# Kernel tuning notes

Measured on AMD Instinct MI355X. Metric: run time of the kernel, lower is better.

Reference implementation:

```python
import jax, jax.numpy as jnp
import numpy as np
from jax import lax

B, T, D, H, C, FF, NH = 256, 48, 89, 128, 64, 64, 8
HD = C // NH


def _pos_encoding(n, c):
    pos = jnp.arange(n, dtype=jnp.float32)[:, None]
    div = jnp.exp(jnp.arange(0, c, 2, dtype=jnp.float32) * (-np.log(10000.0) / c))
    pe = jnp.zeros((n, c), dtype=jnp.float32)
    pe = pe.at[:, 0::2].set(jnp.sin(pos * div))
    pe = pe.at[:, 1::2].set(jnp.cos(pos * div))
    return pe


def _ln(x, g, b):
    m = x.mean(-1, keepdims=True)
    v = ((x - m) ** 2).mean(-1, keepdims=True)
    return (x - m) / jnp.sqrt(v + 1e-5) * g + b


def setup_inputs():
    key = jax.random.key(0)
    ks = iter(jax.random.split(key, 64))
    def n(shape, s=0.05):
        return (jax.random.normal(next(ks), shape) * s).astype(jnp.float32)
    x = jax.random.normal(next(ks), (B, T, D), dtype=jnp.float32)
    mask = (jax.random.uniform(next(ks), (B, T, D)) < 0.8).astype(jnp.float32)
    deltas = (jax.random.uniform(next(ks), (B, T, D)) * 5.0).astype(jnp.float32)
    last_obs = jax.random.normal(next(ks), (B, T, D), dtype=jnp.float32)
    medians = (jax.random.uniform(next(ks), (D,)) * 2.0).astype(jnp.float32)
    return dict(
        x=x, mask=mask, deltas=deltas, last_obs=last_obs, medians=medians,
        W_dh=n((H, D)), b_dh=n((H,)), W_dx=n((D, D)), b_dx=n((D,)),
        W_hist=n((D, H)), b_hist=n((D,)), W_feat=n((D, D)), b_feat=n((D,)),
        W_wc=n((D, 2 * D)), b_wc=n((D,)), W_wo=n((D, D)), b_wo=n((D,)),
        W_cls=n((1, H)), b_cls=n((1,)),
        W_ih=n((3 * H, 2 * D)), W_hh=n((3 * H, H)), b_ih=n((3 * H,)), b_hh=n((3 * H,)),
        W_inp=n((C, D)), b_inp=n((C,)), W_op1=n((H, C)), b_op1=n((H,)),
        W_op2=n((2 * T,)), b_op2=n((1,)),
        attn_in_w=n((3 * C, C)), attn_in_b=n((3 * C,)),
        attn_out_w=n((C, C)), attn_out_b=n((C,)),
        ln1_g=jnp.ones((C,)), ln1_b=jnp.zeros((C,)),
        ln2_g=jnp.ones((C,)), ln2_b=jnp.zeros((C,)),
        ff1_w=n((FF, C)), ff1_b=n((FF,)), ff2_w=n((C, FF)), ff2_b=n((C,)))


def _forward(x, mask, deltas, last_obs, medians,
             W_dh, b_dh, W_dx, b_dx, W_hist, b_hist, W_feat, b_feat,
             W_wc, b_wc, W_wo, b_wo, W_cls, b_cls,
             W_ih, W_hh, b_ih, b_hh, W_inp, b_inp, W_op1, b_op1, W_op2, b_op2,
             attn_in_w, attn_in_b, attn_out_w, attn_out_b,
             ln1_g, ln1_b, ln2_g, ln2_b, ff1_w, ff1_b, ff2_w, ff2_b):
    # Decay_obs: weight = 0.5*(1 - tanh(sign(dd)*|linear(dd)|))
    dd = deltas - medians[None, None, :]
    wd = dd @ W_wo.T + b_wo
    decay_factor = 0.5 * (1.0 - jnp.tanh(jnp.sign(dd) * jnp.abs(wd)))

    # time encoder: 1x1 conv projection + positional encoding
    pe = _pos_encoding(T, C)[None]                      # [1,T,C]
    d_lo = last_obs @ W_inp.T + b_inp + pe              # [B,T,C]
    d_df = decay_factor @ W_inp.T + b_inp + pe          # [B,T,C]
    data = jnp.concatenate([d_lo, d_df], axis=1)        # [B,2T,C]

    # torch TransformerEncoderLayer (post-norm, gelu, dropout off).
    # NOTE: layer is NOT batch_first, so attention runs over axis 0 (B);
    # axis 1 (2T) behaves as the batch — faithful to the source.
    qkv = data @ attn_in_w.T + attn_in_b                # [B,2T,3C]
    q, k, v = jnp.split(qkv, 3, axis=-1)
    q = q.reshape(B, 2 * T, NH, HD)
    k = k.reshape(B, 2 * T, NH, HD)
    v = v.reshape(B, 2 * T, NH, HD)
    scores = jnp.einsum('snhd,tnhd->nhst', q, k) / np.sqrt(HD)
    probs = jax.nn.softmax(scores, axis=-1)
    o = jnp.einsum('nhst,tnhd->snhd', probs, v).reshape(B, 2 * T, C)
    o = o @ attn_out_w.T + attn_out_b
    x1 = _ln(data + o, ln1_g, ln1_b)
    ff = jax.nn.gelu(x1 @ ff1_w.T + ff1_b, approximate=False) @ ff2_w.T + ff2_b
    data = _ln(x1 + ff, ln2_g, ln2_b)                   # [B,2T,C]

    data = data @ W_op1.T + b_op1                       # [B,2T,H]
    h0 = jnp.einsum('bnh,n->bh', data, W_op2) + b_op2[0]  # Conv1d(2T->1,k=1)

    diag_w = jnp.diagonal(W_dx)                         # temp_decay_x diag mask
    offdiag = 1.0 - jnp.eye(D, dtype=x.dtype)

    def step(carry, inp):
        h, loss = carry
        x_t, m_t, d_t = inp
        gamma_h = jnp.exp(-jax.nn.relu(d_t @ W_dh.T + b_dh))
        h = h * gamma_h
        x_h = h @ W_hist.T + b_hist
        x_r = m_t * x_t + (1.0 - m_t) * x_h
        xu = x_r @ (W_feat * offdiag).T + b_feat
        gamma_x = jnp.exp(-jax.nn.relu(d_t * diag_w + b_dx))
        beta = jnp.concatenate([gamma_x, m_t], axis=-1) @ W_wc.T + b_wc
        x_comb = beta * xu + (1.0 - beta) * x_h
        loss = loss + jnp.sum(jnp.abs(x_t - x_comb) * m_t) / (jnp.sum(m_t) + 1e-5)
        x_imp_t = m_t * x_t + (1.0 - m_t) * x_comb
        gi = jnp.concatenate([x_imp_t, m_t], axis=-1) @ W_ih.T + b_ih
        gh = h @ W_hh.T + b_hh
        ir, iz, ig = jnp.split(gi, 3, axis=-1)
        hr, hz, hg = jnp.split(gh, 3, axis=-1)
        r = jax.nn.sigmoid(ir + hr)
        z = jax.nn.sigmoid(iz + hz)
        g = jnp.tanh(ig + r * hg)
        h = (1.0 - z) * g + z * h
        return (h, loss), (x_imp_t, h)

    xs = (x.transpose(1, 0, 2), mask.transpose(1, 0, 2), deltas.transpose(1, 0, 2))
    (h, x_loss), (x_imp_T, hid_T) = lax.scan(step, (h0, jnp.zeros((), x.dtype)), xs)
    x_imp = x_imp_T.transpose(1, 0, 2)                  # [B,T,D]
    hiddens = hid_T.transpose(1, 0, 2)                  # [B,T,H]

    y_out = h @ W_cls.T + b_cls
    y_score = jax.nn.sigmoid(y_out)
    return x_imp, x_loss, hiddens, y_out, y_score


def reference(x, mask, deltas, last_obs, medians,
              W_dh, b_dh, W_dx, b_dx, W_hist, b_hist, W_feat, b_feat,
              W_wc, b_wc, W_wo, b_wo, W_cls, b_cls,
              W_ih, W_hh, b_ih, b_hh, W_inp, b_inp, W_op1, b_op1, W_op2, b_op2,
              attn_in_w, attn_in_b, attn_out_w, attn_out_b,
              ln1_g, ln1_b, ln2_g, ln2_b, ff1_w, ff1_b, ff2_w, ff2_b):
    return _forward(x, mask, deltas, last_obs, medians,
                    W_dh, b_dh, W_dx, b_dx, W_hist, b_hist, W_feat, b_feat,
                    W_wc, b_wc, W_wo, b_wo, W_cls, b_cls,
                    W_ih, W_hh, b_ih, b_hh, W_inp, b_inp, W_op1, b_op1, W_op2, b_op2,
                    attn_in_w, attn_in_b, attn_out_w, attn_out_b,
                    ln1_g, ln1_b, ln2_g, ln2_b, ff1_w, ff1_b, ff2_w, ff2_b)
```

## Files before the change

### kernel.cpp

```cpp
#include <hip/hip_runtime.h>
#include <math.h>

#define B_  256
#define T_  48
#define D_  89
#define H_  128
#define C_  64
#define NH_ 8
#define HD_ 8
#define N2T 96

#define XIMP_OFF 0
#define LOSS_OFF 1093632
#define HID_OFF  1093633
#define Y_OFF    2666497
#define YS_OFF   2666753

typedef unsigned int uint_t;

__device__ __forceinline__ float wave_sum64(float v) {
    v += __shfl_xor(v, 32);
    v += __shfl_xor(v, 16);
    v += __shfl_xor(v, 8);
    v += __shfl_xor(v, 4);
    v += __shfl_xor(v, 2);
    v += __shfl_xor(v, 1);
    return v;
}

__device__ __forceinline__ uint_t pack2(float lo, float hi) {
    uint_t a = __float_as_uint(lo), b = __float_as_uint(hi);
    a = (a + 0x7fffu + ((a >> 16) & 1u)) >> 16;
    b = (b + 0x7fffu + ((b >> 16) & 1u)) >> 16;
    return a | (b << 16);
}
__device__ __forceinline__ float blo(uint_t w) { return __uint_as_float(w << 16); }
__device__ __forceinline__ float bhi(uint_t w) { return __uint_as_float(w & 0xffff0000u); }
__device__ __forceinline__ float sigm(float v) { return 1.f / (1.f + __expf(-v)); }

__device__ __forceinline__ void tr_f32(const float* __restrict__ s, float* __restrict__ d,
                                       int li, int R, int C) {
    int r = li / C, c = li - r * C;
    d[c * R + r] = s[li];
}

__global__ void k_prep(const float* W_wo, const float* W_inp, const float* ain_w,
                       const float* aout_w, const float* ff1_w, const float* ff2_w,
                       const float* W_op1,
                       float* W_woT, float* W_inpT, float* ain_T,
                       float* aout_T, float* ff1_T, float* ff2_T, float* op1_T) {
    int i = blockIdx.x * 256 + threadIdx.x;
    if (i < 7921)         tr_f32(W_wo,   W_woT,  i,          89, 89);
    else if (i < 13617)   tr_f32(W_inp,  W_inpT, i - 7921,   64, 89);
    else if (i < 25905)   tr_f32(ain_w,  ain_T,  i - 13617, 192, 64);
    else if (i < 30001)   tr_f32(aout_w, aout_T, i - 25905,  64, 64);
    else if (i < 34097)   tr_f32(ff1_w,  ff1_T,  i - 30001,  64, 64);
    else if (i < 38193)   tr_f32(ff2_w,  ff2_T,  i - 34097,  64, 64);
    else if (i < 46385)   tr_f32(W_op1,  op1_T,  i - 38193, 128, 64);
}

__global__ void k_pack(const float* __restrict__ W_dh, const float* __restrict__ W_hist,
                       const float* __restrict__ W_ih, const float* __restrict__ W_hh,
                       uint_t* __restrict__ wdh_b, uint_t* __restrict__ whist_b,
                       uint_t* __restrict__ wih_b, uint_t* __restrict__ whh_b) {
    int i = blockIdx.x * 256 + threadIdx.x;
    if (i < 5760) {
        int r = i / 45, c = i - r * 45;
        const float* src = W_dh + r * 89;
        float lo = (2 * c < 89) ? src[2 * c] : 0.f;
        float hi = (2 * c + 1 < 89) ? src[2 * c + 1] : 0.f;
        wdh_b[i] = pack2(lo, hi);
    } else if (i < 11456) {
        int j = i - 5760;
        int r = j / 64, c = j - r * 64;
        const float* src = W_hist + r * 128;
        whist_b[j] = pack2(src[2 * c], src[2 * c + 1]);
    } else if (i < 45632) {
        int j = i - 11456;
        int r = j / 89, c = j - r * 89;
        const float* src = W_ih + (size_t)r * 178;
        wih_b[j] = pack2(src[2 * c], src[2 * c + 1]);
    } else if (i < 70208) {
        int j = i - 45632;
        int r = j / 64, c = j - r * 64;
        const float* src = W_hh + (size_t)r * 128;
        whh_b[j] = pack2(src[2 * c], src[2 * c + 1]);
    }
}

__global__ void k_phaseA(const float* __restrict__ last_obs,
                         const float* __restrict__ deltas,
                         const float* __restrict__ medians,
                         const float* __restrict__ W_woT, const float* __restrict__ b_wo,
                         const float* __restrict__ W_inpT, const float* __restrict__ b_inp,
                         float* __restrict__ data) {
    int bt = blockIdx.x;
    int b = bt / T_;
    int t = bt - b * T_;
    __shared__ float dd[D_], lo[D_], dec[D_];
    int tid = threadIdx.x;
    int base = (b * T_ + t) * D_;
    if (tid < D_) {
        float dv = deltas[base + tid] - medians[tid];
        dd[tid] = dv;
        lo[tid] = last_obs[base + tid];
    }
    __syncthreads();
    if (tid < D_) {
        float acc = b_wo[tid];
        for (int j = 0; j < D_; ++j) acc = fmaf(dd[j], W_woT[j * D_ + tid], acc);
        float dv = dd[tid];
        float s = (dv > 0.f) ? 1.f : ((dv < 0.f) ? -1.f : 0.f);
        dec[tid] = 0.5f * (1.f - tanhf(s * fabsf(acc)));
    }
    __syncthreads();
    int c = tid & 63;
    int half = tid >> 6;
    const float* src = half ? dec : lo;
    float acc = b_inp[c];
    for (int j = 0; j < D_; ++j) acc = fmaf(src[j], W_inpT[j * C_ + c], acc);
    int i = c >> 1;
    float div = __expf((float)i * -0.28782313662425574f);
    float ang = (float)t * div;
    float pe = (c & 1) ? cosf(ang) : sinf(ang);
    data[((b * N2T) + half * T_ + t) * C_ + c] = acc + pe;
}

__global__ void k_qkv(const float* __restrict__ data,
                      const float* __restrict__ ain_T, const float* __restrict__ ain_b,
                      float* __restrict__ qb, float* __restrict__ kb, float* __restrict__ vb) {
    int bn = blockIdx.x;
    int s = bn / N2T;
    int n = bn - s * N2T;
    __shared__ float row[C_];
    int tid = threadIdx.x;
    if (tid < C_) row[tid] = data[bn * C_ + tid];
    __syncthreads();
    float acc = ain_b[tid];
    for (int j = 0; j < C_; ++j) acc = fmaf(row[j], ain_T[j * 192 + tid], acc);
    int part = tid >> 6;
    int c = tid & 63;
    int h = c >> 3, d = c & 7;
    float* dst = (part == 0) ? qb : ((part == 1) ? kb : vb);
    dst[(((n * NH_ + h) * B_ + s) * HD_) + d] = acc;
}

__global__ void k_attn(const float* __restrict__ qb, const float* __restrict__ kb,
                       const float* __restrict__ vb, float* __restrict__ attnO) {
    int n = blockIdx.x >> 3;
    int h = blockIdx.x & 7;
    __shared__ float k_lds[B_][HD_ + 1];
    __shared__ float v_lds[B_][HD_ + 1];
    int s = threadIdx.x;
    const float scale = 0.35355339059327373f;
    size_t base = ((size_t)blockIdx.x * B_ + s) * HD_;
    float q[HD_];
    #pragma unroll
    for (int d = 0; d < HD_; ++d) q[d] = qb[base + d] * scale;
    #pragma unroll
    for (int d = 0; d < HD_; ++d) { k_lds[s][d] = kb[base + d]; v_lds[s][d] = vb[base + d]; }
    __syncthreads();
    float m = -1e30f;
    for (int t = 0; t < B_; ++t) {
        float sc = 0.f;
        #pragma unroll
        for (int d = 0; d < HD_; ++d) sc = fmaf(q[d], k_lds[t][d], sc);
        m = fmaxf(m, sc);
    }
    float l = 0.f;
    float acc[HD_] = {0.f, 0.f, 0.f, 0.f, 0.f, 0.f, 0.f, 0.f};
    for (int t = 0; t < B_; ++t) {
        float sc = 0.f;
        #pragma unroll
        for (int d = 0; d < HD_; ++d) sc = fmaf(q[d], k_lds[t][d], sc);
        float p = __expf(sc - m);
        l += p;
        #pragma unroll
        for (int d = 0; d < HD_; ++d) acc[d] = fmaf(p, v_lds[t][d], acc[d]);
    }
    float inv = 1.f / l;
    float* op = attnO + ((size_t)s * N2T + n) * C_ + h * HD_;
    #pragma unroll
    for (int d = 0; d < HD_; ++d) op[d] = acc[d] * inv;
}

__global__ void k_transform(const float* __restrict__ data,
                            const float* __restrict__ attnO,
                            const float* __restrict__ aout_T, const float* __restrict__ aout_b,
                            const float* __restrict__ ln1_g, const float* __restrict__ ln1_b,
                            const float* __restrict__ ff1_T, const float* __restrict__ ff1_b,
                            const float* __restrict__ ff2_T, const float* __restrict__ ff2_b,
                            const float* __restrict__ ln2_g, const float* __restrict__ ln2_b,
                            const float* __restrict__ op1_T, const float* __restrict__ b_op1,
                            float* __restrict__ val) {
    int bn = blockIdx.x;
    __shared__ float orow[C_], x1s[C_], hbuf[C_], x2s[C_];
    int c = threadIdx.x;
    float d0 = data[bn * C_ + c];
    orow[c] = attnO[bn * C_ + c];
    __syncthreads();
    float acc = aout_b[c];
    for (int j = 0; j < C_; ++j) acc = fmaf(orow[j], aout_T[j * C_ + c], acc);
    float r = d0 + acc;
    float mean = wave_sum64(r) * (1.f / 64.f);
    float df = r - mean;
    float var = wave_sum64(df * df) * (1.f / 64.f);
    float x1 = df * rsqrtf(var + 1e-5f) * ln1_g[c] + ln1_b[c];
    x1s[c] = x1;
    __syncthreads();
    acc = ff1_b[c];
    for (int j = 0; j < C_; ++j) acc = fmaf(x1s[j], ff1_T[j * C_ + c], acc);
    float ge = 0.5f * acc * (1.f + erff(acc * 0.7071067811865475f));
    hbuf[c] = ge;
    __syncthreads();
    acc = ff2_b[c];
    for (int j = 0; j < C_; ++j) acc = fmaf(hbuf[j], ff2_T[j * C_ + c], acc);
    float r2 = x1 + acc;
    float mean2 = wave_sum64(r2) * (1.f / 64.f);
    float df2 = r2 - mean2;
    float var2 = wave_sum64(df2 * df2) * (1.f / 64.f);
    float x2 = df2 * rsqrtf(var2 + 1e-5f) * ln2_g[c] + ln2_b[c];
    x2s[c] = x2;
    __syncthreads();
    #pragma unroll
    for (int rep = 0; rep < 2; ++rep) {
        int k = c + rep * 64;
        float a2 = b_op1[k];
        for (int j = 0; j < C_; ++j) a2 = fmaf(x2s[j], op1_T[j * H_ + k], a2);
        val[(size_t)bn * H_ + k] = a2;
    }
}

__global__ void k_reduce_h0(const float* __restrict__ val,
                            const float* __restrict__ W_op2, const float* __restrict__ b_op2,
                            float* __restrict__ h0) {
    int b = blockIdx.x;
    int h = threadIdx.x;
    float acc = b_op2[0];
    for (int n = 0; n < N2T; ++n)
        acc = fmaf(val[((size_t)b * N2T + n) * H_ + h], W_op2[n], acc);
    h0[b * H_ + h] = acc;
}

__global__ void k_den(const float* __restrict__ mask, float* __restrict__ den) {
    int t = blockIdx.x;
    int tid = threadIdx.x;
    float s = 0.f;
    const int total = B_ * D_;
    for (int i = tid; i < total; i += 256) {
        int b = i / D_;
        int d = i - b * D_;
        s += mask[(b * T_ + t) * D_ + d];
    }
    s = wave_sum64(s);
    __shared__ float red[4];
    if ((tid & 63) == 0) red[tid >> 6] = s;
    __syncthreads();
    if (tid == 0) den[t] = red[0] + red[1] + red[2] + red[3];
}

__global__ __launch_bounds__(1024)
void k_scan(const float* __restrict__ x, const float* __restrict__ mask,
            const float* __restrict__ deltas,
            const uint_t* __restrict__ wdh_b, const float* __restrict__ b_dh,
            const float* __restrict__ W_dx, const float* __restrict__ b_dx,
            const uint_t* __restrict__ whist_b, const float* __restrict__ b_hist,
            const float* __restrict__ W_feat, const float* __restrict__ b_feat,
            const float* __restrict__ W_wc, const float* __restrict__ b_wc,
            const uint_t* __restrict__ wih_b, const uint_t* __restrict__ whh_b,
            const float* __restrict__ b_ih, const float* __restrict__ b_hh,
            const float* __restrict__ W_cls, const float* __restrict__ b_cls,
            const float* __restrict__ h0,
            float* __restrict__ out, float* __restrict__ num_part) {
    int b = blockIdx.x;
    int tid = threadIdx.x;
    int wave = tid >> 6;
    int lane = tid & 63;
    int oo = lane >> 3;
    int jj = lane & 7;

    __shared__ __align__(16) float h_s[H_];
    __shared__ __align__(16) float xt_s[96], dt_s[96], xr_s[96], xh_s[96], diff_s[96];
    __shared__ __align__(16) float catg_s[184];
    __shared__ __align__(16) float catb_s[184];
    __shared__ __align__(16) float gis[384], ghs[384];
    __shared__ __align__(16) uint_t wwc_l[7921];
    __shared__ __align__(16) uint_t wfeat_l[4005];

    for (int i = tid; i < 7921; i += 1024) {
        int r = i / 89, c = i - r * 89;
        const float* wr = W_wc + (size_t)r * 178;
        wwc_l[i] = pack2(wr[2 * c], wr[2 * c + 1]);
    }
    for (int i = tid; i < 4005; i += 1024) {
        int r = i / 45, c = i - r * 45;
        const float* wr = W_feat + r * 89;
        float lo = (2 * c == r) ? 0.f : wr[2 * c];
        float hi = (c == 44 || 2 * c + 1 == r) ? 0.f : wr[2 * c + 1];
        wfeat_l[i] = pack2(lo, hi);
    }
    if (tid < 128) h_s[tid] = h0[b * H_ + tid];
    if (tid >= 512 && tid < 519) {
        int l = tid - 512;
        xr_s[89 + l] = 0.f;
        dt_s[89 + l] = 0.f;
    }
    {
        int base = b * T_ * D_;
        if (tid >= 128 && tid < 217) xt_s[tid - 128] = x[base + tid - 128];
        else if (tid >= 224 && tid < 313) {
            float m = mask[base + tid - 224];
            catg_s[89 + tid - 224] = m;
            catb_s[89 + tid - 224] = m;
        }
        else if (tid >= 320 && tid < 409) dt_s[tid - 320] = deltas[base + tid - 320];
    }
    __syncthreads();

    for (int t = 0; t < T_; ++t) {
        {
            int o = wave * 8 + oo;
            const uint_t* wr = wdh_b + o * 45;
            float a0 = 0.f, a1 = 0.f;
            #pragma unroll
            for (int it = 0; it < 5; ++it) {
                int j = jj + 8 * it;
                uint_t w = wr[j];
                float2 dv = *(const float2*)(dt_s + 2 * j);
                a0 = fmaf(blo(w), dv.x, a0);
                a1 = fmaf(bhi(w), dv.y, a1);
            }
            if (jj < 5) {
                int j = 40 + jj;
                uint_t w = wr[j];
                float2 dv = *(const float2*)(dt_s + 2 * j);
                a0 = fmaf(blo(w), dv.x, a0);
                a1 = fmaf(bhi(w), dv.y, a1);
            }
            float acc = a0 + a1;
            acc += __shfl_xor(acc, 1); acc += __shfl_xor(acc, 2); acc += __shfl_xor(acc, 4);
            if (jj == 0) h_s[o] *= __expf(-fmaxf(acc + b_dh[o], 0.f));
        }
        __syncthreads();
        for (int c = wave; c < 60; c += 16) {
            if (c < 12) {
                int o = c * 8 + oo;
                int ro = (o < 89) ? o : 88;
                const uint_t* wr = whist_b + ro * 64;
                float a0 = 0.f, a1 = 0.f;
                #pragma unroll
                for (int it = 0; it < 8; ++it) {
                    int j = jj + 8 * it;
                    uint_t w = wr[j];
                    float2 hv = *(const float2*)(h_s + 2 * j);
                    a0 = fmaf(blo(w), hv.x, a0);
                    a1 = fmaf(bhi(w), hv.y, a1);
                }
                float acc = a0 + a1;
                acc += __shfl_xor(acc, 1); acc += __shfl_xor(acc, 2); acc += __shfl_xor(acc, 4);
                if (jj == 0 && o < 89) {
                    float xh = acc + b_hist[o];
                    xh_s[o] = xh;
                    float m = catb_s[89 + o];
                    xr_s[o] = m * xt_s[o] + (1.f - m) * xh;
                    catb_s[o] = __expf(-fmaxf(dt_s[o] * W_dx[o * 90] + b_dx[o], 0.f));
                }
            } else {
                int o = (c - 12) * 8 + oo;
                const uint_t* wr = whh_b + o * 64;
                float a0 = 0.f, a1 = 0.f;
                #pragma unroll
                for (int it = 0; it < 8; ++it) {
                    int j = jj + 8 * it;
                    uint_t w = wr[j];
                    float2 hv = *(const float2*)(h_s + 2 * j);
                    a0 = fmaf(blo(w), hv.x, a0);
                    a1 = fmaf(bhi(w), hv.y, a1);
                }
                float acc = a0 + a1;
                acc += __shfl_xor(acc, 1); acc += __shfl_xor(acc, 2); acc += __shfl_xor(acc, 4);
                if (jj == 0) ghs[o] = acc + b_hh[o];
            }
        }
        __syncthreads();
        for (int c = wave; c < 12; c += 16) {
            int o = c * 8 + oo;
            int ro = (o < 89) ? o : 88;
            const uint_t* wf = wfeat_l + ro * 45;
            float a0 = 0.f, a1 = 0.f;
            #pragma unroll
            for (int it = 0; it < 5; ++it) {
                int j2 = jj + 8 * it;
                uint_t w = wf[j2];
                float2 xv = *(const float2*)(xr_s + 2 * j2);
                a0 = fmaf(blo(w), xv.x, a0);
                a1 = fmaf(bhi(w), xv.y, a1);
            }
            if (jj < 5) {
                int j2 = 40 + jj;
                uint_t w = wf[j2];
                float2 xv = *(const float2*)(xr_s + 2 * j2);
                a0 = fmaf(blo(w), xv.x, a0);
                a1 = fmaf(bhi(w), xv.y, a1);
            }
            float xu = a0 + a1;
            xu += __shfl_xor(xu, 1); xu += __shfl_xor(xu, 2); xu += __shfl_xor(xu, 4);
            const uint_t* wc = wwc_l + ro * 89;
            float c0 = 0.f, c1 = 0.f;
            #pragma unroll
            for (int it = 0; it < 11; ++it) {
                int j2 = jj + 8 * it;
                uint_t w = wc[j2];
                float2 cv = *(const float2*)(catb_s + 2 * j2);
                c0 = fmaf(blo(w), cv.x, c0);
                c1 = fmaf(bhi(w), cv.y, c1);
            }
            if (jj == 0) {
                uint_t w = wc[88];
                float2 cv = *(const float2*)(catb_s + 176);
                c0 = fmaf(blo(w), cv.x, c0);
                c1 = fmaf(bhi(w), cv.y, c1);
            }
            float bt = c0 + c1;
            bt += __shfl_xor(bt, 1); bt += __shfl_xor(bt, 2); bt += __shfl_xor(bt, 4);
            if (jj == 0 && o < 89) {
                float xuf = xu + b_feat[o];
                float btf = bt + b_wc[o];
                float xc = btf * xuf + (1.f - btf) * xh_s[o];
                float m = catb_s[89 + o];
                float xtv = xt_s[o];
                float xi = m * xtv + (1.f - m) * xc;
                catg_s[o] = xi;
                out[XIMP_OFF + (b * T_ + t) * D_ + o] = xi;
                diff_s[o] = fabsf(xtv - xc) * m;
            }
        }
        __syncthreads();
        for (int c = wave; c < 48; c += 16) {
            int o = c * 8 + oo;
            const uint_t* wr = wih_b + o * 89;
            float a0 = 0.f, a1 = 0.f;
            #pragma unroll
            for (int it = 0; it < 11; ++it) {
                int j = jj + 8 * it;
                uint_t w = wr[j];
                float2 xv = *(const float2*)(catg_s + 2 * j);
                a0 = fmaf(blo(w), xv.x, a0);
                a1 = fmaf(bhi(w), xv.y, a1);
            }
            if (jj == 0) {
                uint_t w = wr[88];
                float2 xv = *(const float2*)(catg_s + 176);
                a0 = fmaf(blo(w), xv.x, a0);
                a1 = fmaf(bhi(w), xv.y, a1);
            }
            float acc = a0 + a1;
            acc += __shfl_xor(acc, 1); acc += __shfl_xor(acc, 2); acc += __shfl_xor(acc, 4);
            if (jj == 0) gis[o] = acc + b_ih[o];
        }
        __syncthreads();
        if (tid < 128) {
            float r = sigm(gis[tid] + ghs[tid]);
            float z = sigm(gis[128 + tid] + ghs[128 + tid]);
            float g = tanhf(gis[256 + tid] + r * ghs[256 + tid]);
            float hn = (1.f - z) * g + z * h_s[tid];
            h_s[tid] = hn;
            out[HID_OFF + (size_t)(b * T_ + t) * H_ + tid] = hn;
        } else if (tid >= 960) {
            int l = tid - 960;
            float s = diff_s[l] + ((l < 25) ? diff_s[64 + l] : 0.f);
            s = wave_sum64(s);
            if (l == 0) num_part[t * B_ + b] = s;
        } else if (t + 1 < T_) {
            int nb = (b * T_ + t + 1) * D_;
            if (tid < 217) xt_s[tid - 128] = x[nb + tid - 128];
            else if (tid >= 224 && tid < 313) {
                float m = mask[nb + tid - 224];
                catg_s[89 + tid - 224] = m;
                catb_s[89 + tid - 224] = m;
            }
            else if (tid >= 320 && tid < 409) dt_s[tid - 320] = deltas[nb + tid - 320];
        }
        __syncthreads();
    }
    if (tid < 64) {
        float p = h_s[tid] * W_cls[tid] + h_s[tid + 64] * W_cls[tid + 64];
        p = wave_sum64(p);
        if (tid == 0) {
            float y = p + b_cls[0];
            out[Y_OFF + b] = y;
            out[YS_OFF + b] = 1.f / (1.f + __expf(-y));
        }
    }
}

__global__ void k_loss(const float* __restrict__ num_part, const float* __restrict__ den,
                       float* __restrict__ out) {
    int tid = threadIdx.x;
    float v = 0.f;
    if (tid < T_) {
        float s = 0.f;
        const float* np_ = num_part + tid * B_;
        for (int b = 0; b < B_; ++b) s += np_[b];
        v = s / (den[tid] + 1e-5f);
    }
    v = wave_sum64(v);
    if (tid == 0) out[LOSS_OFF] = v;
}

extern "C" void kernel_launch(void* const* d_in, const int* in_sizes, int n_in,
                              void* d_out, int out_size, void* d_ws, size_t ws_size,
                              hipStream_t stream) {
    const float* x        = (const float*)d_in[0];
    const float* mask     = (const float*)d_in[1];
    const float* deltas   = (const float*)d_in[2];
    const float* last_obs = (const float*)d_in[3];
    const float* medians  = (const float*)d_in[4];
    const float* W_dh  = (const float*)d_in[5];
    const float* b_dh  = (const float*)d_in[6];
    const float* W_dx  = (const float*)d_in[7];
    const float* b_dx  = (const float*)d_in[8];
    const float* W_hist= (const float*)d_in[9];
    const float* b_hist= (const float*)d_in[10];
    const float* W_feat= (const float*)d_in[11];
    const float* b_feat= (const float*)d_in[12];
    const float* W_wc  = (const float*)d_in[13];
    const float* b_wc  = (const float*)d_in[14];
    const float* W_wo  = (const float*)d_in[15];
    const float* b_wo  = (const float*)d_in[16];
    const float* W_cls = (const float*)d_in[17];
    const float* b_cls = (const float*)d_in[18];
    const float* W_ih  = (const float*)d_in[19];
    const float* W_hh  = (const float*)d_in[20];
    const float* b_ih  = (const float*)d_in[21];
    const float* b_hh  = (const float*)d_in[22];
    const float* W_inp = (const float*)d_in[23];
    const float* b_inp = (const float*)d_in[24];
    const float* W_op1 = (const float*)d_in[25];
    const float* b_op1 = (const float*)d_in[26];
    const float* W_op2 = (const float*)d_in[27];
    const float* b_op2 = (const float*)d_in[28];
    const float* attn_in_w  = (const float*)d_in[29];
    const float* attn_in_b  = (const float*)d_in[30];
    const float* attn_out_w = (const float*)d_in[31];
    const float* attn_out_b = (const float*)d_in[32];
    const float* ln1_g = (const float*)d_in[33];
    const float* ln1_b = (const float*)d_in[34];
    const float* ln2_g = (const float*)d_in[35];
    const float* ln2_b = (const float*)d_in[36];
    const float* ff1_w = (const float*)d_in[37];
    const float* ff1_b = (const float*)d_in[38];
    const float* ff2_w = (const float*)d_in[39];
    const float* ff2_b = (const float*)d_in[40];

    float* out = (float*)d_out;
    float* ws = (float*)d_ws;

    float* data  = ws;
    float* qb    = data  + (size_t)B_ * N2T * C_;
    float* kb    = qb    + (size_t)N2T * NH_ * B_ * HD_;
    float* vb    = kb    + (size_t)N2T * NH_ * B_ * HD_;
    float* attnO = vb    + (size_t)N2T * NH_ * B_ * HD_;
    float* val   = attnO + (size_t)B_ * N2T * C_;
    float* h0    = val   + (size_t)B_ * N2T * H_;
    float* den   = h0    + (size_t)B_ * H_;
    float* nump  = den   + 64;
    float* W_woT = nump  + T_ * B_;
    float* W_inpT= W_woT + 7921;
    float* ain_T = W_inpT + 5696;
    float* aout_T= ain_T + 12288;
    float* ff1_T = aout_T + 4096;
    float* ff2_T = ff1_T + 4096;
    float* op1_T = ff2_T + 4096;
    uint_t* wdh_b   = (uint_t*)(op1_T + 8192);
    uint_t* whist_b = wdh_b + 5760;
    uint_t* wih_b   = whist_b + 5696;
    uint_t* whh_b   = wih_b + 34176;

    k_prep<<<182, 256, 0, stream>>>(W_wo, W_inp, attn_in_w, attn_out_w, ff1_w, ff2_w, W_op1,
                                    W_woT, W_inpT, ain_T, aout_T, ff1_T, ff2_T, op1_T);
    k_pack<<<275, 256, 0, stream>>>(W_dh, W_hist, W_ih, W_hh, wdh_b, whist_b, wih_b, whh_b);
    k_phaseA<<<B_ * T_, 128, 0, stream>>>(last_obs, deltas, medians, W_woT, b_wo, W_inpT, b_inp, data);
    k_qkv<<<B_ * N2T, 192, 0, stream>>>(data, ain_T, attn_in_b, qb, kb, vb);
    k_attn<<<N2T * NH_, 256, 0, stream>>>(qb, kb, vb, attnO);
    k_transform<<<B_ * N2T, 64, 0, stream>>>(data, attnO, aout_T, attn_out_b,
                                             ln1_g, ln1_b, ff1_T, ff1_b, ff2_T, ff2_b,
                                             ln2_g, ln2_b, op1_T, b_op1, val);
    k_reduce_h0<<<B_, H_, 0, stream>>>(val, W_op2, b_op2, h0);
    k_den<<<T_, 256, 0, stream>>>(mask, den);
    k_scan<<<B_, 1024, 0, stream>>>(x, mask, deltas,
                                    wdh_b, b_dh, W_dx, b_dx, whist_b, b_hist, W_feat, b_feat,
                                    W_wc, b_wc, wih_b, whh_b, b_ih, b_hh, W_cls, b_cls,
                                    h0, out, nump);
    k_loss<<<1, 64, 0, stream>>>(nump, den, out);
}
```

Before: 625.9 us.

## Hoist mask/gamma-dependent GEMVs off the recurrence critical path in scan

The W_wc (beta) and the mask half of W_ih products depend only on the current step's mask and deltas, not on the hidden state. They now run in the first phase of each step, alongside the decay GEMV, instead of in the later serial phases. The gamma_x decay is computed while loading the next step's deltas. The later phases then only do the half-width W_ih product on the imputed values, shortening the dependent chain per timestep. The cost is more work in the first phase and a split W_ih layout with padding.

```diff
diff --git a/kernel.cpp b/kernel.cpp
--- a/kernel.cpp
+++ b/kernel.cpp
@@ -62,7 +62,8 @@
 __global__ void k_pack(const float* __restrict__ W_dh, const float* __restrict__ W_hist,
                        const float* __restrict__ W_ih, const float* __restrict__ W_hh,
                        uint_t* __restrict__ wdh_b, uint_t* __restrict__ whist_b,
-                       uint_t* __restrict__ wih_b, uint_t* __restrict__ whh_b) {
+                       uint_t* __restrict__ wihx_b, uint_t* __restrict__ wihm_b,
+                       uint_t* __restrict__ whh_b) {
     int i = blockIdx.x * 256 + threadIdx.x;
     if (i < 5760) {
         int r = i / 45, c = i - r * 45;
@@ -75,13 +76,22 @@
         int r = j / 64, c = j - r * 64;
         const float* src = W_hist + r * 128;
         whist_b[j] = pack2(src[2 * c], src[2 * c + 1]);
-    } else if (i < 45632) {
+    } else if (i < 28736) {
         int j = i - 11456;
-        int r = j / 89, c = j - r * 89;
+        int r = j / 45, c = j - r * 45;
         const float* src = W_ih + (size_t)r * 178;
-        wih_b[j] = pack2(src[2 * c], src[2 * c + 1]);
-    } else if (i < 70208) {
-        int j = i - 45632;
+        float lo = src[2 * c];
+        float hi = (2 * c + 1 < 89) ? src[2 * c + 1] : 0.f;
+        wihx_b[j] = pack2(lo, hi);
+    } else if (i < 46016) {
+        int j = i - 28736;
+        int r = j / 45, c = j - r * 45;
+        const float* src = W_ih + (size_t)r * 178 + 89;
+        float lo = src[2 * c];
+        float hi = (2 * c + 1 < 89) ? src[2 * c + 1] : 0.f;
+        wihm_b[j] = pack2(lo, hi);
+    } else if (i < 70592) {
+        int j = i - 46016;
         int r = j / 64, c = j - r * 64;
         const float* src = W_hh + (size_t)r * 128;
         whh_b[j] = pack2(src[2 * c], src[2 * c + 1]);
@@ -267,7 +277,8 @@
             const uint_t* __restrict__ whist_b, const float* __restrict__ b_hist,
             const float* __restrict__ W_feat, const float* __restrict__ b_feat,
             const float* __restrict__ W_wc, const float* __restrict__ b_wc,
-            const uint_t* __restrict__ wih_b, const uint_t* __restrict__ whh_b,
+            const uint_t* __restrict__ wihx_b, const uint_t* __restrict__ wihm_b,
+            const uint_t* __restrict__ whh_b,
             const float* __restrict__ b_ih, const float* __restrict__ b_hh,
             const float* __restrict__ W_cls, const float* __restrict__ b_cls,
             const float* __restrict__ h0,
@@ -280,66 +291,131 @@
     int jj = lane & 7;
 
     __shared__ __align__(16) float h_s[H_];
-    __shared__ __align__(16) float xt_s[96], dt_s[96], xr_s[96], xh_s[96], diff_s[96];
-    __shared__ __align__(16) float catg_s[184];
-    __shared__ __align__(16) float catb_s[184];
+    __shared__ __align__(16) float xt_s[96], dt_s[96], xr_s[96], xh_s[96];
+    __shared__ __align__(16) float m_s[96], gx_s[96], ximp_s[96], beta_s[96], diff_s[96];
     __shared__ __align__(16) float gis[384], ghs[384];
-    __shared__ __align__(16) uint_t wwc_l[7921];
+    __shared__ __align__(16) uint_t wwcg_l[4005];
+    __shared__ __align__(16) uint_t wwcm_l[4005];
     __shared__ __align__(16) uint_t wfeat_l[4005];
 
-    for (int i = tid; i < 7921; i += 1024) {
-        int r = i / 89, c = i - r * 89;
-        const float* wr = W_wc + (size_t)r * 178;
-        wwc_l[i] = pack2(wr[2 * c], wr[2 * c + 1]);
-    }
+    float dxw = 0.f, dxb = 0.f;
+    if (tid >= 320 && tid < 409) {
+        int o = tid - 320;
+        dxw = W_dx[o * 90];
+        dxb = b_dx[o];
+    }
+
     for (int i = tid; i < 4005; i += 1024) {
         int r = i / 45, c = i - r * 45;
-        const float* wr = W_feat + r * 89;
-        float lo = (2 * c == r) ? 0.f : wr[2 * c];
-        float hi = (c == 44 || 2 * c + 1 == r) ? 0.f : wr[2 * c + 1];
-        wfeat_l[i] = pack2(lo, hi);
+        const float* wr = W_wc + (size_t)r * 178;
+        float lo = wr[2 * c];
+        float hi = (2 * c + 1 < 89) ? wr[2 * c + 1] : 0.f;
+        wwcg_l[i] = pack2(lo, hi);
+        const float* wm = wr + 89;
+        float lo2 = wm[2 * c];
+        float hi2 = (2 * c + 1 < 89) ? wm[2 * c + 1] : 0.f;
+        wwcm_l[i] = pack2(lo2, hi2);
+        const float* wf = W_feat + r * 89;
+        float lo3 = (2 * c == r) ? 0.f : wf[2 * c];
+        float hi3 = (2 * c + 1 >= 89 || 2 * c + 1 == r) ? 0.f : wf[2 * c + 1];
+        wfeat_l[i] = pack2(lo3, hi3);
     }
     if (tid < 128) h_s[tid] = h0[b * H_ + tid];
-    if (tid >= 512 && tid < 519) {
-        int l = tid - 512;
-        xr_s[89 + l] = 0.f;
-        dt_s[89 + l] = 0.f;
+    if (tid >= 416 && tid < 419) {
+        int l = tid - 416;
+        dt_s[89 + l] = 0.f; xr_s[89 + l] = 0.f; m_s[89 + l] = 0.f;
+        gx_s[89 + l] = 0.f; ximp_s[89 + l] = 0.f;
     }
     {
         int base = b * T_ * D_;
         if (tid >= 128 && tid < 217) xt_s[tid - 128] = x[base + tid - 128];
-        else if (tid >= 224 && tid < 313) {
-            float m = mask[base + tid - 224];
-            catg_s[89 + tid - 224] = m;
-            catb_s[89 + tid - 224] = m;
+        else if (tid >= 224 && tid < 313) m_s[tid - 224] = mask[base + tid - 224];
+        else if (tid >= 320 && tid < 409) {
+            int o = tid - 320;
+            float dv = deltas[base + o];
+            dt_s[o] = dv;
+            gx_s[o] = __expf(-fmaxf(dv * dxw + dxb, 0.f));
         }
-        else if (tid >= 320 && tid < 409) dt_s[tid - 320] = deltas[base + tid - 320];
     }
     __syncthreads();
 
     for (int t = 0; t < T_; ++t) {
-        {
-            int o = wave * 8 + oo;
-            const uint_t* wr = wdh_b + o * 45;
-            float a0 = 0.f, a1 = 0.f;
-            #pragma unroll
-            for (int it = 0; it < 5; ++it) {
-                int j = jj + 8 * it;
-                uint_t w = wr[j];
-                float2 dv = *(const float2*)(dt_s + 2 * j);
-                a0 = fmaf(blo(w), dv.x, a0);
-                a1 = fmaf(bhi(w), dv.y, a1);
-            }
-            if (jj < 5) {
-                int j = 40 + jj;
-                uint_t w = wr[j];
-                float2 dv = *(const float2*)(dt_s + 2 * j);
-                a0 = fmaf(blo(w), dv.x, a0);
-                a1 = fmaf(bhi(w), dv.y, a1);
-            }
-            float acc = a0 + a1;
-            acc += __shfl_xor(acc, 1); acc += __shfl_xor(acc, 2); acc += __shfl_xor(acc, 4);
-            if (jj == 0) h_s[o] *= __expf(-fmaxf(acc + b_dh[o], 0.f));
+        for (int c = wave; c < 76; c += 16) {
+            if (c < 16) {
+                int o = c * 8 + oo;
+                const uint_t* wr = wdh_b + o * 45;
+                float a0 = 0.f, a1 = 0.f;
+                #pragma unroll
+                for (int it = 0; it < 5; ++it) {
+                    int j = jj + 8 * it;
+                    uint_t w = wr[j];
+                    float2 dv = *(const float2*)(dt_s + 2 * j);
+                    a0 = fmaf(blo(w), dv.x, a0);
+                    a1 = fmaf(bhi(w), dv.y, a1);
+                }
+                if (jj < 5) {
+                    int j = 40 + jj;
+                    uint_t w = wr[j];
+                    float2 dv = *(const float2*)(dt_s + 2 * j);
+                    a0 = fmaf(blo(w), dv.x, a0);
+                    a1 = fmaf(bhi(w), dv.y, a1);
+                }
+                float acc = a0 + a1;
+                acc += __shfl_xor(acc, 1); acc += __shfl_xor(acc, 2); acc += __shfl_xor(acc, 4);
+                if (jj == 0) h_s[o] *= __expf(-fmaxf(acc + b_dh[o], 0.f));
+            } else if (c < 28) {
+                int o = (c - 16) * 8 + oo;
+                int ro = (o < 89) ? o : 88;
+                const uint_t* wg = wwcg_l + ro * 45;
+                const uint_t* wm = wwcm_l + ro * 45;
+                float a0 = 0.f, a1 = 0.f;
+                #pragma unroll
+                for (int it = 0; it < 5; ++it) {
+                    int j = jj + 8 * it;
+                    uint_t w1 = wg[j], w2 = wm[j];
+                    float2 gv = *(const float2*)(gx_s + 2 * j);
+                    float2 mv = *(const float2*)(m_s + 2 * j);
+                    a0 = fmaf(blo(w1), gv.x, a0);
+                    a1 = fmaf(bhi(w1), gv.y, a1);
+                    a0 = fmaf(blo(w2), mv.x, a0);
+                    a1 = fmaf(bhi(w2), mv.y, a1);
+                }
+                if (jj < 5) {
+                    int j = 40 + jj;
+                    uint_t w1 = wg[j], w2 = wm[j];
+                    float2 gv = *(const float2*)(gx_s + 2 * j);
+                    float2 mv = *(const float2*)(m_s + 2 * j);
+                    a0 = fmaf(blo(w1), gv.x, a0);
+                    a1 = fmaf(bhi(w1), gv.y, a1);
+                    a0 = fmaf(blo(w2), mv.x, a0);
+                    a1 = fmaf(bhi(w2), mv.y, a1);
+                }
+                float acc = a0 + a1;
+                acc += __shfl_xor(acc, 1); acc += __shfl_xor(acc, 2); acc += __shfl_xor(acc, 4);
+                if (jj == 0 && o < 89) beta_s[o] = acc + b_wc[o];
+            } else {
+                int o = (c - 28) * 8 + oo;
+                const uint_t* wr = wihm_b + o * 45;
+                float a0 = 0.f, a1 = 0.f;
+                #pragma unroll
+                for (int it = 0; it < 5; ++it) {
+                    int j = jj + 8 * it;
+                    uint_t w = wr[j];
+                    float2 mv = *(const float2*)(m_s + 2 * j);
+                    a0 = fmaf(blo(w), mv.x, a0);
+                    a1 = fmaf(bhi(w), mv.y, a1);
+                }
+                if (jj < 5) {
+                    int j = 40 + jj;
+                    uint_t w = wr[j];
+                    float2 mv = *(const float2*)(m_s + 2 * j);
+                    a0 = fmaf(blo(w), mv.x, a0);
+                    a1 = fmaf(bhi(w), mv.y, a1);
+                }
+                float acc = a0 + a1;
+                acc += __shfl_xor(acc, 1); acc += __shfl_xor(acc, 2); acc += __shfl_xor(acc, 4);
+                if (jj == 0) gis[o] = acc + b_ih[o];
+            }
         }
         __syncthreads();
         for (int c = wave; c < 60; c += 16) {
@@ -361,9 +437,8 @@
                 if (jj == 0 && o < 89) {
                     float xh = acc + b_hist[o];
                     xh_s[o] = xh;
-                    float m = catb_s[89 + o];
+                    float m = m_s[o];
                     xr_s[o] = m * xt_s[o] + (1.f - m) * xh;
-                    catb_s[o] = __expf(-fmaxf(dt_s[o] * W_dx[o * 90] + b_dx[o], 0.f));
                 }
             } else {
                 int o = (c - 12) * 8 + oo;
@@ -390,47 +465,29 @@
             float a0 = 0.f, a1 = 0.f;
             #pragma unroll
             for (int it = 0; it < 5; ++it) {
-                int j2 = jj + 8 * it;
-                uint_t w = wf[j2];
-                float2 xv = *(const float2*)(xr_s + 2 * j2);
+                int j = jj + 8 * it;
+                uint_t w = wf[j];
+                float2 xv = *(const float2*)(xr_s + 2 * j);
                 a0 = fmaf(blo(w), xv.x, a0);
                 a1 = fmaf(bhi(w), xv.y, a1);
             }
             if (jj < 5) {
-                int j2 = 40 + jj;
-                uint_t w = wf[j2];
-                float2 xv = *(const float2*)(xr_s + 2 * j2);
+                int j = 40 + jj;
+                uint_t w = wf[j];
+                float2 xv = *(const float2*)(xr_s + 2 * j);
                 a0 = fmaf(blo(w), xv.x, a0);
                 a1 = fmaf(bhi(w), xv.y, a1);
             }
             float xu = a0 + a1;
             xu += __shfl_xor(xu, 1); xu += __shfl_xor(xu, 2); xu += __shfl_xor(xu, 4);
-            const uint_t* wc = wwc_l + ro * 89;
-            float c0 = 0.f, c1 = 0.f;
-            #pragma unroll
-            for (int it = 0; it < 11; ++it) {
-                int j2 = jj + 8 * it;
-                uint_t w = wc[j2];
-                float2 cv = *(const float2*)(catb_s + 2 * j2);
-                c0 = fmaf(blo(w), cv.x, c0);
-                c1 = fmaf(bhi(w), cv.y, c1);
-            }
-            if (jj == 0) {
-                uint_t w = wc[88];
-                float2 cv = *(const float2*)(catb_s + 176);
-                c0 = fmaf(blo(w), cv.x, c0);
-                c1 = fmaf(bhi(w), cv.y, c1);
-            }
-            float bt = c0 + c1;
-            bt += __shfl_xor(bt, 1); bt += __shfl_xor(bt, 2); bt += __shfl_xor(bt, 4);
             if (jj == 0 && o < 89) {
                 float xuf = xu + b_feat[o];
-                float btf = bt + b_wc[o];
+                float btf = beta_s[o];
                 float xc = btf * xuf + (1.f - btf) * xh_s[o];
-                float m = catb_s[89 + o];
+                float m = m_s[o];
                 float xtv = xt_s[o];
                 float xi = m * xtv + (1.f - m) * xc;
-                catg_s[o] = xi;
+                ximp_s[o] = xi;
                 out[XIMP_OFF + (b * T_ + t) * D_ + o] = xi;
                 diff_s[o] = fabsf(xtv - xc) * m;
             }
@@ -438,25 +495,26 @@
         __syncthreads();
         for (int c = wave; c < 48; c += 16) {
             int o = c * 8 + oo;
-            const uint_t* wr = wih_b + o * 89;
+            const uint_t* wr = wihx_b + o * 45;
             float a0 = 0.f, a1 = 0.f;
             #pragma unroll
-            for (int it = 0; it < 11; ++it) {
+            for (int it = 0; it < 5; ++it) {
                 int j = jj + 8 * it;
                 uint_t w = wr[j];
-                float2 xv = *(const float2*)(catg_s + 2 * j);
+                float2 xv = *(const float2*)(ximp_s + 2 * j);
                 a0 = fmaf(blo(w), xv.x, a0);
                 a1 = fmaf(bhi(w), xv.y, a1);
             }
-            if (jj == 0) {
-                uint_t w = wr[88];
-                float2 xv = *(const float2*)(catg_s + 176);
+            if (jj < 5) {
+                int j = 40 + jj;
+                uint_t w = wr[j];
+                float2 xv = *(const float2*)(ximp_s + 2 * j);
                 a0 = fmaf(blo(w), xv.x, a0);
                 a1 = fmaf(bhi(w), xv.y, a1);
             }
             float acc = a0 + a1;
             acc += __shfl_xor(acc, 1); acc += __shfl_xor(acc, 2); acc += __shfl_xor(acc, 4);
-            if (jj == 0) gis[o] = acc + b_ih[o];
+            if (jj == 0) gis[o] += acc;
         }
         __syncthreads();
         if (tid < 128) {
@@ -474,12 +532,13 @@
         } else if (t + 1 < T_) {
             int nb = (b * T_ + t + 1) * D_;
             if (tid < 217) xt_s[tid - 128] = x[nb + tid - 128];
-            else if (tid >= 224 && tid < 313) {
-                float m = mask[nb + tid - 224];
-                catg_s[89 + tid - 224] = m;
-                catb_s[89 + tid - 224] = m;
-            }
-            else if (tid >= 320 && tid < 409) dt_s[tid - 320] = deltas[nb + tid - 320];
+            else if (tid >= 224 && tid < 313) m_s[tid - 224] = mask[nb + tid - 224];
+            else if (tid >= 320 && tid < 409) {
+                int o = tid - 320;
+                float dv = deltas[nb + o];
+                dt_s[o] = dv;
+                gx_s[o] = __expf(-fmaxf(dv * dxw + dxb, 0.f));
+            }
         }
         __syncthreads();
     }
@@ -574,12 +633,14 @@
     float* op1_T = ff2_T + 4096;
     uint_t* wdh_b   = (uint_t*)(op1_T + 8192);
     uint_t* whist_b = wdh_b + 5760;
-    uint_t* wih_b   = whist_b + 5696;
-    uint_t* whh_b   = wih_b + 34176;
+    uint_t* wihx_b  = whist_b + 5696;
+    uint_t* wihm_b  = wihx_b + 17280;
+    uint_t* whh_b   = wihm_b + 17280;
 
     k_prep<<<182, 256, 0, stream>>>(W_wo, W_inp, attn_in_w, attn_out_w, ff1_w, ff2_w, W_op1,
                                     W_woT, W_inpT, ain_T, aout_T, ff1_T, ff2_T, op1_T);
-    k_pack<<<275, 256, 0, stream>>>(W_dh, W_hist, W_ih, W_hh, wdh_b, whist_b, wih_b, whh_b);
+    k_pack<<<276, 256, 0, stream>>>(W_dh, W_hist, W_ih, W_hh,
+                                    wdh_b, whist_b, wihx_b, wihm_b, whh_b);
     k_phaseA<<<B_ * T_, 128, 0, stream>>>(last_obs, deltas, medians, W_woT, b_wo, W_inpT, b_inp, data);
     k_qkv<<<B_ * N2T, 192, 0, stream>>>(data, ain_T, attn_in_b, qb, kb, vb);
     k_attn<<<N2T * NH_, 256, 0, stream>>>(qb, kb, vb, attnO);
@@ -590,7 +651,7 @@
     k_den<<<T_, 256, 0, stream>>>(mask, den);
     k_scan<<<B_, 1024, 0, stream>>>(x, mask, deltas,
                                     wdh_b, b_dh, W_dx, b_dx, whist_b, b_hist, W_feat, b_feat,
-                                    W_wc, b_wc, wih_b, whh_b, b_ih, b_hh, W_cls, b_cls,
+                                    W_wc, b_wc, wihx_b, wihm_b, whh_b, b_ih, b_hh, W_cls, b_cls,
                                     h0, out, nump);
     k_loss<<<1, 64, 0, stream>>>(nump, den, out);
 }
```

Result: no change. 625.5 us (-0.1%).
